# Kernel tuning notes

Measured on AMD Instinct MI355X. Metric: run time of the kernel, lower is better.

Reference implementation:

```python
import jax, jax.numpy as jnp
import numpy as np

NTA = 65536   # total atoms across all crystals
NC = 1024     # number of crystals
NO = 256      # descriptor output dim (desc.NO)
H = 332       # int(NO * 1.3) hidden dim of per-species MLP
S = 4         # number of species


def setup_inputs() -> dict:
    key = jax.random.key(0)
    ks = jax.random.split(key, 8)
    symbols = jax.random.randint(ks[0], (NTA,), 0, S)
    positions = jax.random.normal(ks[1], (NTA, 3), jnp.float32) * 3.0
    cells = jax.random.normal(ks[2], (NC, 3, 3), jnp.float32)
    pbcs = jnp.ones((NC, 3), dtype=bool)
    energyidx = jnp.arange(NC)
    crystalidx = jax.random.randint(ks[3], (NTA,), 0, NC)
    # stand-in descriptor projection (replaces external REANN desc module)
    Wd = jax.random.normal(ks[4], (3, NO), jnp.float32) * 0.5
    # stacked per-species MLP params: Linear(NO,H) -> SiLU -> Linear(H,1)
    W1 = jax.random.normal(ks[5], (S, NO, H), jnp.float32) / np.sqrt(NO).astype(np.float32)
    b1 = jnp.zeros((S, H), jnp.float32)
    W2 = jax.random.normal(ks[6], (S, H), jnp.float32) / np.sqrt(H).astype(np.float32)
    b2 = jnp.zeros((S,), jnp.float32)
    return {
        "symbols": symbols, "positions": positions, "cells": cells,
        "pbcs": pbcs, "energyidx": energyidx, "crystalidx": crystalidx,
        "Wd": Wd, "W1": W1, "b1": b1, "W2": W2, "b2": b2,
    }


def _atomic_energies(positions, symbols, Wd, W1, b1, W2, b2):
    # stand-in descriptor: [NTA, NO]
    feat = jnp.tanh(positions @ Wd)
    n_species = W1.shape[0]
    e = jnp.zeros((positions.shape[0],), feat.dtype)
    # species-routed small MLPs: dense compute + select (fixed small loop over species)
    for s in range(n_species):
        h = jax.nn.silu(feat @ W1[s] + b1[s])       # [NTA, H]
        es = h @ W2[s] + b2[s]                      # [NTA]
        e = jnp.where(symbols == s, es, e)
    return e


def reference(symbols, positions, cells, pbcs, energyidx, crystalidx, Wd, W1, b1, W2, b2):
    num_crystals = energyidx.shape[0]

    def total_energy(pos):
        en = _atomic_energies(pos, symbols, Wd, W1, b1, W2, b2)   # [NTA]
        E = jax.ops.segment_sum(en, crystalidx, num_segments=num_crystals)  # [NC]
        return jnp.sum(E), (en, E)

    # torch code: forces = grad(sum(energy), positions)  (positive gradient)
    forces, (energies, energy) = jax.grad(total_energy, has_aux=True)(positions)
    return (energies, energy, forces)
```

## Files before the change

kernel.cpp:

```cpp
#include <hip/hip_runtime.h>

#define NTA 65536
#define NC 1024
#define NO 256
#define HDIM 332
#define HP 352
#define NSP 4
#define NOUT (NTA + NC + NTA*3)
#define SORT_CAP (NTA + 256)

#define DP_STRIDE 720
#define LDS_MAIN  49152

typedef __attribute__((ext_vector_type(8))) short short8;
typedef __attribute__((ext_vector_type(4))) float f32x4;

#define OFF_CNT   0
#define OFF_CUR   64
#define OFF_START 128
#define OFF_FLAG  160
#define OFF_SORT  256
#define OFF_B1P   263680
#define OFF_W2P   269312
#define OFF_W1T   274944
#define OFF_W1P   995840
#define OFF_FACC  1716736

__device__ __forceinline__ unsigned short f2bf(float f){
  unsigned int u = __builtin_bit_cast(unsigned int, f);
  u += 0x7fffu + ((u>>16)&1u);
  return (unsigned short)(u>>16);
}
__device__ __forceinline__ float bf2f(unsigned short h){
  unsigned int u = ((unsigned int)h)<<16;
  return __builtin_bit_cast(float, u);
}
__device__ __forceinline__ float ldf(const void* p, int idx, int isbf){
  if (isbf) return bf2f(((const unsigned short*)p)[idx]);
  return ((const float*)p)[idx];
}
__device__ __forceinline__ float rcpf(float x){ return __builtin_amdgcn_rcpf(x); }

__global__ void k_init(float* __restrict__ acc, unsigned int* __restrict__ wshead,
                       int* __restrict__ sorted, const unsigned short* __restrict__ posu,
                       unsigned int* __restrict__ flag){
  int i = blockIdx.x*256 + threadIdx.x;
  acc[i] = 0.f;
  if (i < 32) wshead[i] = 0u;
  if (i < SORT_CAP) sorted[i] = -1;
  if (blockIdx.x == 1027 && threadIdx.x < 64){
    unsigned short u = posu[2*threadIdx.x];
    int e = (u>>7)&0xFF;
    bool inr = (e >= 110 && e <= 140);
    unsigned long long m = __ballot(inr);
    if (threadIdx.x == 0) flag[0] = (__popcll(m) >= 32) ? 1u : 0u;
  }
}

__global__ void k_count(const int* __restrict__ sym, unsigned int* __restrict__ cnt){
  __shared__ unsigned int h[NSP];
  int t = threadIdx.x;
  if (t < NSP) h[t] = 0u;
  __syncthreads();
  int i = blockIdx.x*256 + t;
  atomicAdd(&h[sym[i]], 1u);
  __syncthreads();
  if (t < NSP) atomicAdd(&cnt[t], h[t]);
}

__global__ void k_starts(const unsigned int* __restrict__ cnt, int* __restrict__ starts){
  if (threadIdx.x == 0){
    int a = 0; starts[0] = 0;
    for (int s=0;s<NSP;s++){ a += (int)(((cnt[s]+63u)>>6)<<6); starts[s+1] = a; }
  }
}

__global__ void k_scatter(const int* __restrict__ sym, const int* __restrict__ starts,
                          unsigned int* __restrict__ cur, int* __restrict__ sorted){
  int i = blockIdx.x*256 + threadIdx.x;
  int s = sym[i];
  int lane = threadIdx.x & 63;
  #pragma unroll
  for (int ss=0; ss<NSP; ss++){
    unsigned long long m = __ballot(s==ss);
    if (s == ss){
      int leader = __builtin_ctzll(m);
      int cw = __popcll(m);
      unsigned int b = 0;
      if (lane == leader) b = atomicAdd(&cur[ss], (unsigned int)cw);
      b = (unsigned int)__shfl((int)b, leader);
      int rank = __popcll(m & ((1ull<<lane) - 1ull));
      sorted[starts[ss] + (int)b + rank] = i;
    }
  }
}

__global__ void k_prepw(const void* __restrict__ W1, const void* __restrict__ b1,
                        const void* __restrict__ W2, const unsigned int* __restrict__ flag,
                        unsigned short* __restrict__ w1t, unsigned short* __restrict__ w1p,
                        float* __restrict__ b1p, float* __restrict__ w2p){
  const int isbf = (int)flag[0];
  int idx = blockIdx.x*256 + threadIdx.x;
  int s = idx / (HP*NO);
  int r = idx % (HP*NO);
  int j = r / NO;
  int i = r % NO;
  float v = (j < HDIM) ? ldf(W1, (s*NO + i)*HDIM + j, isbf) : 0.f;
  unsigned short hv = f2bf(v);
  w1t[(s*HP + j)*NO + i] = hv;
  w1p[(s*NO + i)*HP + j] = hv;
  if (i == 0){
    b1p[s*HP + j] = (j < HDIM) ? ldf(b1, s*HDIM + j, isbf) : 0.f;
    w2p[s*HP + j] = (j < HDIM) ? ldf(W2, s*HDIM + j, isbf) : 0.f;
  }
}

__global__ __launch_bounds__(256,3) void k_main(
    const int* __restrict__ sorted, const int* __restrict__ starts,
    const void* __restrict__ pos, const void* __restrict__ Wd,
    const unsigned short* __restrict__ W1T, const unsigned short* __restrict__ W1P,
    const float* __restrict__ b1p, const float* __restrict__ w2p,
    const void* __restrict__ b2g, const int* __restrict__ crys,
    const unsigned int* __restrict__ flag,
    float* __restrict__ Eatom, float* __restrict__ Ecry, float* __restrict__ forces)
{
  extern __shared__ char smem[];
  ushort4* wdT = (ushort4*)smem;
  char* featB  = smem + 2048;
  char* dpB    = smem + 2048;
  float* Fpart = (float*)(smem + 2048);
  float* Epart = (float*)(smem + 48128);

  const int base = blockIdx.x*64;
  if (base >= starts[4]) return;
  const int isbf = (int)flag[0];
  int sp = 0;
  #pragma unroll
  for (int s=1;s<NSP;s++) sp = (base >= starts[s]) ? s : sp;

  const int tid = threadIdx.x;
  const int l = tid & 63;
  const int w = tid >> 6;
  const int c = l & 15;
  const int g = l >> 4;

  {
    float x = ldf(Wd, tid, isbf), y = ldf(Wd, NO+tid, isbf), z = ldf(Wd, 2*NO+tid, isbf);
    ushort4 u; u.x = f2bf(x); u.y = f2bf(y); u.z = f2bf(z); u.w = 0;
    wdT[tid] = u;
  }
  __syncthreads();

  {
    const int m = l;
    int a = sorted[base + m];
    float px=0.f, py=0.f, pz=0.f;
    if (a >= 0){ px = ldf(pos,3*a,isbf); py = ldf(pos,3*a+1,isbf); pz = ldf(pos,3*a+2,isbf); }
    const int swz = (m&7)<<4;
    char* rowp = featB + m*512;
    #pragma unroll
    for (int k8=0;k8<8;k8++){
      int i0 = w*64 + k8*8;
      unsigned int pk[4];
      #pragma unroll
      for (int p2=0;p2<4;p2++){
        unsigned short hv[2];
        #pragma unroll
        for (int e2=0;e2<2;e2++){
          ushort4 wv = wdT[i0 + 2*p2 + e2];
          float v = px*bf2f(wv.x) + py*bf2f(wv.y) + pz*bf2f(wv.z);
          float e = __expf(2.f*v);
          hv[e2] = f2bf(1.f - 2.f*rcpf(e+1.f));
        }
        pk[p2] = (unsigned int)hv[0] | ((unsigned int)hv[1]<<16);
      }
      *(uint4*)(rowp + ((i0*2) ^ swz)) = make_uint4(pk[0],pk[1],pk[2],pk[3]);
    }
  }
  __syncthreads();

  const unsigned short* W1Ts = W1T + sp*HP*NO;
  const float* b1s = b1p + sp*HP;
  const float* w2s = w2p + sp*HP;
  const int nT1 = (w==3) ? 4 : 6;
  float esp[4] = {0.f,0.f,0.f,0.f};
  uint2 dpk[2][3][4];

  #pragma unroll
  for (int pass=0; pass<2; pass++){
    f32x4 acc[3][4];
    #pragma unroll
    for (int t=0;t<3;t++)
      #pragma unroll
      for (int nb=0;nb<4;nb++) acc[t][nb] = f32x4{0.f,0.f,0.f,0.f};

    #pragma unroll
    for (int kk=0; kk<8; kk++){
      short8 bfr[4];
      #pragma unroll
      for (int nb=0;nb<4;nb++){
        int m = nb*16 + c;
        bfr[nb] = *(const short8*)(featB + m*512 + ((kk*64 + g*16) ^ ((m&7)<<4)));
      }
      #pragma unroll
      for (int t=0;t<3;t++){
        int tt = pass*3 + t;
        if (tt < nT1){
          const short8 afr = *(const short8*)((const char*)W1Ts + ((6*w+tt)*16 + c)*512 + kk*64 + g*16);
          #pragma unroll
          for (int nb=0;nb<4;nb++)
            acc[t][nb] = __builtin_amdgcn_mfma_f32_16x16x32_bf16(afr, bfr[nb], acc[t][nb], 0,0,0);
        }
      }
    }
    #pragma unroll
    for (int t=0;t<3;t++){
      int tt = pass*3 + t;
      if (tt < nT1){
        const int j0 = (6*w+tt)*16 + g*4;
        const float4 b1v = *(const float4*)(b1s + j0);
        const float4 w2v = *(const float4*)(w2s + j0);
        const float* b1a = (const float*)&b1v;
        const float* w2a = (const float*)&w2v;
        #pragma unroll
        for (int nb=0;nb<4;nb++){
          unsigned short dph[4];
          #pragma unroll
          for (int q=0;q<4;q++){
            float pre = acc[t][nb][q] + b1a[q];
            float sg = rcpf(1.f + __expf(-pre));
            float h = pre*sg;
            esp[nb] += h*w2a[q];
            float dsl = sg*(1.f + pre*(1.f - sg));
            dph[q] = f2bf(w2a[q]*dsl);
          }
          dpk[pass][t][nb] = make_uint2((unsigned)dph[0] | ((unsigned)dph[1]<<16),
                                        (unsigned)dph[2] | ((unsigned)dph[3]<<16));
        }
      }
    }
  }
  #pragma unroll
  for (int nb=0;nb<4;nb++){
    float e = esp[nb];
    e += __shfl_xor(e, 16);
    e += __shfl_xor(e, 32);
    if (g == 0) Epart[w*64 + nb*16 + c] = e;
  }
  __syncthreads();

  #pragma unroll
  for (int pass=0; pass<2; pass++){
    #pragma unroll
    for (int t=0;t<3;t++){
      int tt = pass*3 + t;
      if (tt < nT1){
        const int j0 = (6*w+tt)*16 + g*4;
        #pragma unroll
        for (int nb=0;nb<4;nb++){
          const int m = nb*16 + c;
          *(uint2*)(dpB + m*DP_STRIDE + j0*2) = dpk[pass][t][nb];
        }
      }
    }
  }
  __syncthreads();

  const unsigned short* W1Ps = W1P + sp*NO*HP;
  f32x4 acc2[4][4];
  #pragma unroll
  for (int t2=0;t2<4;t2++)
    #pragma unroll
    for (int nb=0;nb<4;nb++) acc2[t2][nb] = f32x4{0.f,0.f,0.f,0.f};

  #pragma unroll
  for (int kk=0; kk<11; kk++){
    short8 bfr[4];
    #pragma unroll
    for (int nb=0;nb<4;nb++){
      int m = nb*16 + c;
      bfr[nb] = *(const short8*)(dpB + m*DP_STRIDE + kk*64 + g*16);
    }
    #pragma unroll
    for (int t2=0;t2<4;t2++){
      const short8 afr = *(const short8*)((const char*)W1Ps + ((4*w+t2)*16 + c)*704 + kk*64 + g*16);
      #pragma unroll
      for (int nb=0;nb<4;nb++)
        acc2[t2][nb] = __builtin_amdgcn_mfma_f32_16x16x32_bf16(afr, bfr[nb], acc2[t2][nb], 0,0,0);
    }
  }

  int a4[4]; float px4[4], py4[4], pz4[4];
  #pragma unroll
  for (int nb=0;nb<4;nb++){
    int aa = sorted[base + nb*16 + c];
    a4[nb] = aa;
    float x=0.f,y=0.f,z=0.f;
    if (aa >= 0){ x=ldf(pos,3*aa,isbf); y=ldf(pos,3*aa+1,isbf); z=ldf(pos,3*aa+2,isbf); }
    px4[nb]=x; py4[nb]=y; pz4[nb]=z;
  }
  float fax[4] = {0.f,0.f,0.f,0.f};
  float fay[4] = {0.f,0.f,0.f,0.f};
  float faz[4] = {0.f,0.f,0.f,0.f};
  #pragma unroll
  for (int t2=0;t2<4;t2++){
    const int i0 = (4*w+t2)*16 + g*4;
    #pragma unroll
    for (int q=0;q<4;q++){
      ushort4 wv = wdT[i0 + q];
      float wx = bf2f(wv.x), wy = bf2f(wv.y), wz = bf2f(wv.z);
      #pragma unroll
      for (int nb=0;nb<4;nb++){
        float v = px4[nb]*wx + py4[nb]*wy + pz4[nb]*wz;
        float e = __expf(2.f*v);
        float f = 1.f - 2.f*rcpf(e+1.f);
        float gsc = acc2[t2][nb][q] * (1.f - f*f);
        fax[nb] += gsc*wx;
        fay[nb] += gsc*wy;
        faz[nb] += gsc*wz;
      }
    }
  }
  #pragma unroll
  for (int nb=0;nb<4;nb++){
    float x = fax[nb], y = fay[nb], z = faz[nb];
    x += __shfl_xor(x, 16); x += __shfl_xor(x, 32);
    y += __shfl_xor(y, 16); y += __shfl_xor(y, 32);
    z += __shfl_xor(z, 16); z += __shfl_xor(z, 32);
    fax[nb] = x; fay[nb] = y; faz[nb] = z;
  }
  __syncthreads();
  #pragma unroll
  for (int nb=0;nb<4;nb++){
    if (g == 0){
      const int m = nb*16 + c;
      Fpart[w*192 + m*3 + 0] = fax[nb];
      Fpart[w*192 + m*3 + 1] = fay[nb];
      Fpart[w*192 + m*3 + 2] = faz[nb];
    }
  }
  __syncthreads();

  if (w == 0){
    int a = sorted[base + l];
    if (a >= 0){
      float E = Epart[l] + Epart[64+l] + Epart[128+l] + Epart[192+l]
              + ldf(b2g, sp, isbf);
      Eatom[a] = E;
      atomicAdd(&Ecry[crys[a]], E);
      float fx = 0.f, fy = 0.f, fz = 0.f;
      #pragma unroll
      for (int ww=0; ww<4; ww++){
        fx += Fpart[ww*192 + l*3 + 0];
        fy += Fpart[ww*192 + l*3 + 1];
        fz += Fpart[ww*192 + l*3 + 2];
      }
      forces[3*a+0] = fx;
      forces[3*a+1] = fy;
      forces[3*a+2] = fz;
    }
  }
}

__global__ void k_out(const float* __restrict__ Eatom, const float* __restrict__ Ecry,
                      const float* __restrict__ Facc, float* __restrict__ out){
  int i = blockIdx.x*256 + threadIdx.x;
  float v;
  if (i < NTA)            v = Eatom[i];
  else if (i < NTA + NC)  v = Ecry[i - NTA];
  else                    v = Facc[i - NTA - NC];
  out[i] = v;
}

extern "C" void kernel_launch(void* const* d_in, const int* in_sizes, int n_in,
                              void* d_out, int out_size, void* d_ws, size_t ws_size,
                              hipStream_t stream) {
  const int*   symbols    = (const int*)  d_in[0];
  const void*  positions  = d_in[1];
  const int*   crystalidx = (const int*)  d_in[5];
  const void*  Wd         = d_in[6];
  const void*  W1         = d_in[7];
  const void*  b1         = d_in[8];
  const void*  W2         = d_in[9];
  const void*  b2         = d_in[10];
  float* dout = (float*)d_out;

  char* ws = (char*)d_ws;
  unsigned int* cnt    = (unsigned int*)(ws + OFF_CNT);
  unsigned int* cur    = (unsigned int*)(ws + OFF_CUR);
  int*          starts = (int*)         (ws + OFF_START);
  unsigned int* flag   = (unsigned int*)(ws + OFF_FLAG);
  int*          sorted = (int*)         (ws + OFF_SORT);
  float*        b1p    = (float*)       (ws + OFF_B1P);
  float*        w2p    = (float*)       (ws + OFF_W2P);
  unsigned short* w1t  = (unsigned short*)(ws + OFF_W1T);
  unsigned short* w1pp = (unsigned short*)(ws + OFF_W1P);
  float*        Facc   = (float*)       (ws + OFF_FACC);
  float*        Eatom  = Facc + NTA*3;
  float*        Ecry   = Eatom + NTA;

  hipFuncSetAttribute((const void*)k_main,
                      hipFuncAttributeMaxDynamicSharedMemorySize, LDS_MAIN);

  k_init   <<<1028,256, 0, stream>>>(Facc, (unsigned int*)ws, sorted,
                                     (const unsigned short*)positions, flag);
  k_count  <<<256, 256, 0, stream>>>(symbols, cnt);
  k_starts <<<1,    64, 0, stream>>>(cnt, starts);
  k_scatter<<<256, 256, 0, stream>>>(symbols, starts, cur, sorted);
  k_prepw  <<<1408,256, 0, stream>>>(W1, b1, W2, flag, w1t, w1pp, b1p, w2p);
  k_main   <<<1028,256, LDS_MAIN, stream>>>(sorted, starts, positions, Wd,
                                            w1t, w1pp, b1p, w2p, b2, crystalidx,
                                            flag, Eatom, Ecry, Facc);
  k_out    <<<1028,256, 0, stream>>>(Eatom, Ecry, Facc, dout);
}
```

Baseline: 165.0 us.

## Use six waves in main kernel, fuse prep kernels, tile weight transpose

The main kernel moves from 4 to 6 waves per block. The first GEMM now runs in a single pass that writes the swizzled activation derivative straight to LDS, instead of holding it in registers across two passes. The count, starts and init kernels are merged into fewer launches plus memsets, and the W1 transpose goes through an LDS tile to get coalesced stores. The goal is more parallelism per block, less register pressure and fewer launches, at the cost of more LDS per block and a grid that only zeroes the small accumulators.

After: 190.4 us. +15.4%, slower.

```diff
diff --git a/kernel.cpp b/kernel.cpp
--- a/kernel.cpp
+++ b/kernel.cpp
@@ -7,10 +7,10 @@
 #define HP 352
 #define NSP 4
 #define NOUT (NTA + NC + NTA*3)
-#define SORT_CAP (NTA + 256)
-
-#define DP_STRIDE 720
-#define LDS_MAIN  49152
+#define SORT_CAP (NTA + 4*64)
+
+#define DP_STRIDE 768
+#define LDS_MAIN  57344
 
 typedef __attribute__((ext_vector_type(8))) short short8;
 typedef __attribute__((ext_vector_type(4))) float f32x4;
@@ -25,6 +25,7 @@
 #define OFF_W1T   274944
 #define OFF_W1P   995840
 #define OFF_FACC  1716736
+#define OFF_ECRY  2765312
 
 __device__ __forceinline__ unsigned short f2bf(float f){
   unsigned int u = __builtin_bit_cast(unsigned int, f);
@@ -41,45 +42,45 @@
 }
 __device__ __forceinline__ float rcpf(float x){ return __builtin_amdgcn_rcpf(x); }
 
-__global__ void k_init(float* __restrict__ acc, unsigned int* __restrict__ wshead,
-                       int* __restrict__ sorted, const unsigned short* __restrict__ posu,
-                       unsigned int* __restrict__ flag){
-  int i = blockIdx.x*256 + threadIdx.x;
-  acc[i] = 0.f;
-  if (i < 32) wshead[i] = 0u;
+__global__ void k_init2(const int* __restrict__ sym, unsigned int* __restrict__ cnt,
+                        int* __restrict__ sorted, const unsigned short* __restrict__ posu,
+                        unsigned int* __restrict__ flag){
+  __shared__ unsigned int h[NSP];
+  int t = threadIdx.x;
+  if (t < NSP) h[t] = 0u;
+  __syncthreads();
+  int i = blockIdx.x*256 + t;
   if (i < SORT_CAP) sorted[i] = -1;
-  if (blockIdx.x == 1027 && threadIdx.x < 64){
-    unsigned short u = posu[2*threadIdx.x];
+  if (i < NTA) atomicAdd(&h[sym[i]], 1u);
+  __syncthreads();
+  if (t < NSP && h[t]) atomicAdd(&cnt[t], h[t]);
+  if (blockIdx.x == 257 && t < 64){
+    unsigned short u = posu[2*t];
     int e = (u>>7)&0xFF;
     bool inr = (e >= 110 && e <= 140);
     unsigned long long m = __ballot(inr);
-    if (threadIdx.x == 0) flag[0] = (__popcll(m) >= 32) ? 1u : 0u;
-  }
-}
-
-__global__ void k_count(const int* __restrict__ sym, unsigned int* __restrict__ cnt){
-  __shared__ unsigned int h[NSP];
+    if (t == 0) flag[0] = (__popcll(m) >= 32) ? 1u : 0u;
+  }
+}
+
+__global__ void k_scatter2(const int* __restrict__ sym, const unsigned int* __restrict__ cnt,
+                           unsigned int* __restrict__ cur, int* __restrict__ sorted,
+                           int* __restrict__ gstarts){
+  __shared__ int sl[NSP+1];
   int t = threadIdx.x;
-  if (t < NSP) h[t] = 0u;
+  if (t == 0){
+    int a = 0; sl[0] = 0;
+    #pragma unroll
+    for (int s=0;s<NSP;s++){ a += (int)(((cnt[s]+63u)>>6)<<6); sl[s+1] = a; }
+    if (blockIdx.x == 0){
+      #pragma unroll
+      for (int s=0;s<=NSP;s++) gstarts[s] = sl[s];
+    }
+  }
   __syncthreads();
   int i = blockIdx.x*256 + t;
-  atomicAdd(&h[sym[i]], 1u);
-  __syncthreads();
-  if (t < NSP) atomicAdd(&cnt[t], h[t]);
-}
-
-__global__ void k_starts(const unsigned int* __restrict__ cnt, int* __restrict__ starts){
-  if (threadIdx.x == 0){
-    int a = 0; starts[0] = 0;
-    for (int s=0;s<NSP;s++){ a += (int)(((cnt[s]+63u)>>6)<<6); starts[s+1] = a; }
-  }
-}
-
-__global__ void k_scatter(const int* __restrict__ sym, const int* __restrict__ starts,
-                          unsigned int* __restrict__ cur, int* __restrict__ sorted){
-  int i = blockIdx.x*256 + threadIdx.x;
   int s = sym[i];
-  int lane = threadIdx.x & 63;
+  int lane = t & 63;
   #pragma unroll
   for (int ss=0; ss<NSP; ss++){
     unsigned long long m = __ballot(s==ss);
@@ -90,32 +91,52 @@
       if (lane == leader) b = atomicAdd(&cur[ss], (unsigned int)cw);
       b = (unsigned int)__shfl((int)b, leader);
       int rank = __popcll(m & ((1ull<<lane) - 1ull));
-      sorted[starts[ss] + (int)b + rank] = i;
-    }
-  }
-}
-
-__global__ void k_prepw(const void* __restrict__ W1, const void* __restrict__ b1,
-                        const void* __restrict__ W2, const unsigned int* __restrict__ flag,
-                        unsigned short* __restrict__ w1t, unsigned short* __restrict__ w1p,
-                        float* __restrict__ b1p, float* __restrict__ w2p){
+      sorted[sl[ss] + (int)b + rank] = i;
+    }
+  }
+}
+
+__global__ void k_prepw2(const void* __restrict__ W1, const void* __restrict__ b1,
+                         const void* __restrict__ W2, const unsigned int* __restrict__ flag,
+                         unsigned short* __restrict__ w1t, unsigned short* __restrict__ w1p,
+                         float* __restrict__ b1p, float* __restrict__ w2p){
+  __shared__ unsigned short T[32][36];
   const int isbf = (int)flag[0];
-  int idx = blockIdx.x*256 + threadIdx.x;
-  int s = idx / (HP*NO);
-  int r = idx % (HP*NO);
-  int j = r / NO;
-  int i = r % NO;
-  float v = (j < HDIM) ? ldf(W1, (s*NO + i)*HDIM + j, isbf) : 0.f;
-  unsigned short hv = f2bf(v);
-  w1t[(s*HP + j)*NO + i] = hv;
-  w1p[(s*NO + i)*HP + j] = hv;
-  if (i == 0){
+  const int bid = blockIdx.x;
+  const int s  = bid / 88;
+  const int jt = (bid % 88) / 8;
+  const int it = bid % 8;
+  const int t = threadIdx.x;
+  {
+    const int il = t >> 3;
+    const int j4 = (t & 7) * 4;
+    const int i = it*32 + il;
+    #pragma unroll
+    for (int e=0;e<4;e++){
+      int j = jt*32 + j4 + e;
+      float v = (j < HDIM) ? ldf(W1, (s*NO + i)*HDIM + j, isbf) : 0.f;
+      T[il][j4+e] = f2bf(v);
+    }
+  }
+  __syncthreads();
+  {
+    const int jl = t >> 3;
+    const int i4 = (t & 7) * 4;
+    ushort4 v; v.x = T[i4][jl]; v.y = T[i4+1][jl]; v.z = T[i4+2][jl]; v.w = T[i4+3][jl];
+    *(ushort4*)&w1t[(s*HP + jt*32 + jl)*NO + it*32 + i4] = v;
+    const int il = t >> 3;
+    const int j4 = (t & 7) * 4;
+    ushort4 u; u.x = T[il][j4]; u.y = T[il][j4+1]; u.z = T[il][j4+2]; u.w = T[il][j4+3];
+    *(ushort4*)&w1p[(s*NO + it*32 + il)*HP + jt*32 + j4] = u;
+  }
+  if (it == 0 && t < 32){
+    int j = jt*32 + t;
     b1p[s*HP + j] = (j < HDIM) ? ldf(b1, s*HDIM + j, isbf) : 0.f;
     w2p[s*HP + j] = (j < HDIM) ? ldf(W2, s*HDIM + j, isbf) : 0.f;
   }
 }
 
-__global__ __launch_bounds__(256,3) void k_main(
+__global__ __launch_bounds__(384,3) void k_main(
     const int* __restrict__ sorted, const int* __restrict__ starts,
     const void* __restrict__ pos, const void* __restrict__ Wd,
     const unsigned short* __restrict__ W1T, const unsigned short* __restrict__ W1P,
@@ -128,8 +149,8 @@
   ushort4* wdT = (ushort4*)smem;
   char* featB  = smem + 2048;
   char* dpB    = smem + 2048;
-  float* Fpart = (float*)(smem + 2048);
-  float* Epart = (float*)(smem + 48128);
+  float* Epart = (float*)(smem + 51200);
+  float* Fpart = (float*)(smem + 52736);
 
   const int base = blockIdx.x*64;
   if (base >= starts[4]) return;
@@ -144,23 +165,24 @@
   const int c = l & 15;
   const int g = l >> 4;
 
-  {
+  if (tid < 256){
     float x = ldf(Wd, tid, isbf), y = ldf(Wd, NO+tid, isbf), z = ldf(Wd, 2*NO+tid, isbf);
     ushort4 u; u.x = f2bf(x); u.y = f2bf(y); u.z = f2bf(z); u.w = 0;
     wdT[tid] = u;
   }
   __syncthreads();
 
-  {
-    const int m = l;
+  for (int u = tid; u < 512; u += 384){
+    const int m = u >> 3;
+    const int q = u & 7;
     int a = sorted[base + m];
     float px=0.f, py=0.f, pz=0.f;
     if (a >= 0){ px = ldf(pos,3*a,isbf); py = ldf(pos,3*a+1,isbf); pz = ldf(pos,3*a+2,isbf); }
     const int swz = (m&7)<<4;
     char* rowp = featB + m*512;
     #pragma unroll
-    for (int k8=0;k8<8;k8++){
-      int i0 = w*64 + k8*8;
+    for (int p4=0;p4<4;p4++){
+      int i0 = q*32 + p4*8;
       unsigned int pk[4];
       #pragma unroll
       for (int p2=0;p2<4;p2++){
@@ -180,63 +202,61 @@
   __syncthreads();
 
   const unsigned short* W1Ts = W1T + sp*HP*NO;
+  const int fr0 = (w<4) ? w*4 : 16 + (w-4)*3;
+  const int nT  = (w<4) ? 4 : 3;
+  f32x4 acc[4][4];
+  #pragma unroll
+  for (int t=0;t<4;t++)
+    #pragma unroll
+    for (int nb=0;nb<4;nb++) acc[t][nb] = f32x4{0.f,0.f,0.f,0.f};
+
+  #pragma unroll
+  for (int kk=0; kk<8; kk++){
+    short8 bfr[4];
+    #pragma unroll
+    for (int nb=0;nb<4;nb++){
+      int m = nb*16 + c;
+      bfr[nb] = *(const short8*)(featB + m*512 + ((kk*64 + g*16) ^ ((m&7)<<4)));
+    }
+    #pragma unroll
+    for (int t=0;t<4;t++){
+      if (t < nT){
+        const short8 afr = *(const short8*)((const char*)W1Ts + ((fr0+t)*16 + c)*512 + kk*64 + g*16);
+        #pragma unroll
+        for (int nb=0;nb<4;nb++)
+          acc[t][nb] = __builtin_amdgcn_mfma_f32_16x16x32_bf16(afr, bfr[nb], acc[t][nb], 0,0,0);
+      }
+    }
+  }
+  __syncthreads();
+
   const float* b1s = b1p + sp*HP;
   const float* w2s = w2p + sp*HP;
-  const int nT1 = (w==3) ? 4 : 6;
   float esp[4] = {0.f,0.f,0.f,0.f};
-  uint2 dpk[2][3][4];
-
-  #pragma unroll
-  for (int pass=0; pass<2; pass++){
-    f32x4 acc[3][4];
-    #pragma unroll
-    for (int t=0;t<3;t++)
-      #pragma unroll
-      for (int nb=0;nb<4;nb++) acc[t][nb] = f32x4{0.f,0.f,0.f,0.f};
-
-    #pragma unroll
-    for (int kk=0; kk<8; kk++){
-      short8 bfr[4];
+  #pragma unroll
+  for (int t=0;t<4;t++){
+    if (t < nT){
+      const int j0 = (fr0+t)*16 + g*4;
+      const float4 b1v = *(const float4*)(b1s + j0);
+      const float4 w2v = *(const float4*)(w2s + j0);
+      const float* b1a = (const float*)&b1v;
+      const float* w2a = (const float*)&w2v;
       #pragma unroll
       for (int nb=0;nb<4;nb++){
-        int m = nb*16 + c;
-        bfr[nb] = *(const short8*)(featB + m*512 + ((kk*64 + g*16) ^ ((m&7)<<4)));
-      }
-      #pragma unroll
-      for (int t=0;t<3;t++){
-        int tt = pass*3 + t;
-        if (tt < nT1){
-          const short8 afr = *(const short8*)((const char*)W1Ts + ((6*w+tt)*16 + c)*512 + kk*64 + g*16);
-          #pragma unroll
-          for (int nb=0;nb<4;nb++)
-            acc[t][nb] = __builtin_amdgcn_mfma_f32_16x16x32_bf16(afr, bfr[nb], acc[t][nb], 0,0,0);
+        const int m = nb*16 + c;
+        unsigned short dph[4];
+        #pragma unroll
+        for (int q=0;q<4;q++){
+          float pre = acc[t][nb][q] + b1a[q];
+          float sg = rcpf(1.f + __expf(-pre));
+          float h = pre*sg;
+          esp[nb] += h*w2a[q];
+          float dsl = sg*(1.f + pre*(1.f - sg));
+          dph[q] = f2bf(w2a[q]*dsl);
         }
-      }
-    }
-    #pragma unroll
-    for (int t=0;t<3;t++){
-      int tt = pass*3 + t;
-      if (tt < nT1){
-        const int j0 = (6*w+tt)*16 + g*4;
-        const float4 b1v = *(const float4*)(b1s + j0);
-        const float4 w2v = *(const float4*)(w2s + j0);
-        const float* b1a = (const float*)&b1v;
-        const float* w2a = (const float*)&w2v;
-        #pragma unroll
-        for (int nb=0;nb<4;nb++){
-          unsigned short dph[4];
-          #pragma unroll
-          for (int q=0;q<4;q++){
-            float pre = acc[t][nb][q] + b1a[q];
-            float sg = rcpf(1.f + __expf(-pre));
-            float h = pre*sg;
-            esp[nb] += h*w2a[q];
-            float dsl = sg*(1.f + pre*(1.f - sg));
-            dph[q] = f2bf(w2a[q]*dsl);
-          }
-          dpk[pass][t][nb] = make_uint2((unsigned)dph[0] | ((unsigned)dph[1]<<16),
-                                        (unsigned)dph[2] | ((unsigned)dph[3]<<16));
-        }
+        *(uint2*)(dpB + m*DP_STRIDE + ((j0*2) ^ ((m&7)<<4))) =
+            make_uint2((unsigned)dph[0] | ((unsigned)dph[1]<<16),
+                       (unsigned)dph[2] | ((unsigned)dph[3]<<16));
       }
     }
   }
@@ -249,27 +269,12 @@
   }
   __syncthreads();
 
-  #pragma unroll
-  for (int pass=0; pass<2; pass++){
-    #pragma unroll
-    for (int t=0;t<3;t++){
-      int tt = pass*3 + t;
-      if (tt < nT1){
-        const int j0 = (6*w+tt)*16 + g*4;
-        #pragma unroll
-        for (int nb=0;nb<4;nb++){
-          const int m = nb*16 + c;
-          *(uint2*)(dpB + m*DP_STRIDE + j0*2) = dpk[pass][t][nb];
-        }
-      }
-    }
-  }
-  __syncthreads();
-
   const unsigned short* W1Ps = W1P + sp*NO*HP;
-  f32x4 acc2[4][4];
-  #pragma unroll
-  for (int t2=0;t2<4;t2++)
+  const int fr2 = (w<4) ? w*3 : 12 + (w-4)*2;
+  const int nT2 = (w<4) ? 3 : 2;
+  f32x4 acc2[3][4];
+  #pragma unroll
+  for (int t2=0;t2<3;t2++)
     #pragma unroll
     for (int nb=0;nb<4;nb++) acc2[t2][nb] = f32x4{0.f,0.f,0.f,0.f};
 
@@ -279,14 +284,16 @@
     #pragma unroll
     for (int nb=0;nb<4;nb++){
       int m = nb*16 + c;
-      bfr[nb] = *(const short8*)(dpB + m*DP_STRIDE + kk*64 + g*16);
-    }
-    #pragma unroll
-    for (int t2=0;t2<4;t2++){
-      const short8 afr = *(const short8*)((const char*)W1Ps + ((4*w+t2)*16 + c)*704 + kk*64 + g*16);
-      #pragma unroll
-      for (int nb=0;nb<4;nb++)
-        acc2[t2][nb] = __builtin_amdgcn_mfma_f32_16x16x32_bf16(afr, bfr[nb], acc2[t2][nb], 0,0,0);
+      bfr[nb] = *(const short8*)(dpB + m*DP_STRIDE + ((kk*64 + g*16) ^ ((m&7)<<4)));
+    }
+    #pragma unroll
+    for (int t2=0;t2<3;t2++){
+      if (t2 < nT2){
+        const short8 afr = *(const short8*)((const char*)W1Ps + ((fr2+t2)*16 + c)*704 + kk*64 + g*16);
+        #pragma unroll
+        for (int nb=0;nb<4;nb++)
+          acc2[t2][nb] = __builtin_amdgcn_mfma_f32_16x16x32_bf16(afr, bfr[nb], acc2[t2][nb], 0,0,0);
+      }
     }
   }
 
@@ -303,21 +310,23 @@
   float fay[4] = {0.f,0.f,0.f,0.f};
   float faz[4] = {0.f,0.f,0.f,0.f};
   #pragma unroll
-  for (int t2=0;t2<4;t2++){
-    const int i0 = (4*w+t2)*16 + g*4;
-    #pragma unroll
-    for (int q=0;q<4;q++){
-      ushort4 wv = wdT[i0 + q];
-      float wx = bf2f(wv.x), wy = bf2f(wv.y), wz = bf2f(wv.z);
+  for (int t2=0;t2<3;t2++){
+    if (t2 < nT2){
+      const int i0 = (fr2+t2)*16 + g*4;
       #pragma unroll
-      for (int nb=0;nb<4;nb++){
-        float v = px4[nb]*wx + py4[nb]*wy + pz4[nb]*wz;
-        float e = __expf(2.f*v);
-        float f = 1.f - 2.f*rcpf(e+1.f);
-        float gsc = acc2[t2][nb][q] * (1.f - f*f);
-        fax[nb] += gsc*wx;
-        fay[nb] += gsc*wy;
-        faz[nb] += gsc*wz;
+      for (int q=0;q<4;q++){
+        ushort4 wv = wdT[i0 + q];
+        float wx = bf2f(wv.x), wy = bf2f(wv.y), wz = bf2f(wv.z);
+        #pragma unroll
+        for (int nb=0;nb<4;nb++){
+          float v = px4[nb]*wx + py4[nb]*wy + pz4[nb]*wz;
+          float e = __expf(2.f*v);
+          float f = 1.f - 2.f*rcpf(e+1.f);
+          float gsc = acc2[t2][nb][q] * (1.f - f*f);
+          fax[nb] += gsc*wx;
+          fay[nb] += gsc*wy;
+          faz[nb] += gsc*wz;
+        }
       }
     }
   }
@@ -327,34 +336,29 @@
     x += __shfl_xor(x, 16); x += __shfl_xor(x, 32);
     y += __shfl_xor(y, 16); y += __shfl_xor(y, 32);
     z += __shfl_xor(z, 16); z += __shfl_xor(z, 32);
-    fax[nb] = x; fay[nb] = y; faz[nb] = z;
-  }
-  __syncthreads();
-  #pragma unroll
-  for (int nb=0;nb<4;nb++){
     if (g == 0){
       const int m = nb*16 + c;
-      Fpart[w*192 + m*3 + 0] = fax[nb];
-      Fpart[w*192 + m*3 + 1] = fay[nb];
-      Fpart[w*192 + m*3 + 2] = faz[nb];
-    }
-  }
-  __syncthreads();
-
-  if (w == 0){
-    int a = sorted[base + l];
+      Fpart[w*192 + m*3 + 0] = x;
+      Fpart[w*192 + m*3 + 1] = y;
+      Fpart[w*192 + m*3 + 2] = z;
+    }
+  }
+  __syncthreads();
+
+  if (tid < 64){
+    int a = sorted[base + tid];
     if (a >= 0){
-      float E = Epart[l] + Epart[64+l] + Epart[128+l] + Epart[192+l]
-              + ldf(b2g, sp, isbf);
+      float E = ldf(b2g, sp, isbf);
+      float fx = 0.f, fy = 0.f, fz = 0.f;
+      #pragma unroll
+      for (int ww=0; ww<6; ww++){
+        E  += Epart[ww*64 + tid];
+        fx += Fpart[ww*192 + tid*3 + 0];
+        fy += Fpart[ww*192 + tid*3 + 1];
+        fz += Fpart[ww*192 + tid*3 + 2];
+      }
       Eatom[a] = E;
       atomicAdd(&Ecry[crys[a]], E);
-      float fx = 0.f, fy = 0.f, fz = 0.f;
-      #pragma unroll
-      for (int ww=0; ww<4; ww++){
-        fx += Fpart[ww*192 + l*3 + 0];
-        fy += Fpart[ww*192 + l*3 + 1];
-        fz += Fpart[ww*192 + l*3 + 2];
-      }
       forces[3*a+0] = fx;
       forces[3*a+1] = fy;
       forces[3*a+2] = fz;
@@ -397,19 +401,19 @@
   unsigned short* w1pp = (unsigned short*)(ws + OFF_W1P);
   float*        Facc   = (float*)       (ws + OFF_FACC);
   float*        Eatom  = Facc + NTA*3;
-  float*        Ecry   = Eatom + NTA;
+  float*        Ecry   = (float*)       (ws + OFF_ECRY);
 
   hipFuncSetAttribute((const void*)k_main,
                       hipFuncAttributeMaxDynamicSharedMemorySize, LDS_MAIN);
 
-  k_init   <<<1028,256, 0, stream>>>(Facc, (unsigned int*)ws, sorted,
-                                     (const unsigned short*)positions, flag);
-  k_count  <<<256, 256, 0, stream>>>(symbols, cnt);
-  k_starts <<<1,    64, 0, stream>>>(cnt, starts);
-  k_scatter<<<256, 256, 0, stream>>>(symbols, starts, cur, sorted);
-  k_prepw  <<<1408,256, 0, stream>>>(W1, b1, W2, flag, w1t, w1pp, b1p, w2p);
-  k_main   <<<1028,256, LDS_MAIN, stream>>>(sorted, starts, positions, Wd,
-                                            w1t, w1pp, b1p, w2p, b2, crystalidx,
-                                            flag, Eatom, Ecry, Facc);
-  k_out    <<<1028,256, 0, stream>>>(Eatom, Ecry, Facc, dout);
-}
+  hipMemsetAsync(ws, 0, 256, stream);
+  hipMemsetAsync(ws + OFF_ECRY, 0, NC*4, stream);
+  k_init2   <<<258, 256, 0, stream>>>(symbols, cnt, sorted,
+                                      (const unsigned short*)positions, flag);
+  k_scatter2<<<256, 256, 0, stream>>>(symbols, cnt, cur, sorted, starts);
+  k_prepw2  <<<352, 256, 0, stream>>>(W1, b1, W2, flag, w1t, w1pp, b1p, w2p);
+  k_main    <<<1028,384, LDS_MAIN, stream>>>(sorted, starts, positions, Wd,
+                                             w1t, w1pp, b1p, w2p, b2, crystalidx,
+                                             flag, Eatom, Ecry, Facc);
+  k_out     <<<1028,256, 0, stream>>>(Eatom, Ecry, Facc, dout);
+}
```
